# Kernel tuning notes

Hardware: AMD Instinct MI355X
Metric: run time of the kernel (lower is better)

The kernel has to match this reference:

```python
import jax, jax.numpy as jnp
import numpy as np

B, S, D, H = 2, 2048, 2048, 32
HD = D // H  # head_dim = 64
ROPE_BASE = 10000.0


def setup_inputs() -> dict:
    key = jax.random.key(0)
    ks = jax.random.split(key, 5)
    x = jax.random.normal(ks[0], (B, S, D), jnp.float32)
    wq = jax.random.normal(ks[1], (D, D), jnp.float32) * 0.02
    wk = jax.random.normal(ks[2], (D, D), jnp.float32) * 0.02
    wv = jax.random.normal(ks[3], (D, D), jnp.float32) * 0.02
    wo = jax.random.normal(ks[4], (D, D), jnp.float32) * 0.02
    # RoPE frequencies, same as llama precompute_freqs_cis: (S, HD//2)
    inv_freq = 1.0 / (ROPE_BASE ** (jnp.arange(0, HD, 2, dtype=jnp.float32) / HD))
    freqs = jnp.outer(jnp.arange(S, dtype=jnp.float32), inv_freq)
    freqs_cos = jnp.cos(freqs)
    freqs_sin = jnp.sin(freqs)
    # additive causal mask (1,1,S,S): 0 on/below diagonal, -1e9 above
    mask = jnp.where(jnp.tril(jnp.ones((S, S), bool)), 0.0, -1e9).astype(jnp.float32)[None, None]
    return {"x": x, "wq": wq, "wk": wk, "wv": wv, "wo": wo,
            "freqs_cos": freqs_cos, "freqs_sin": freqs_sin, "mask": mask}


def _rope(t, cos, sin):
    # t: [b, s, h, d]; cos/sin: [s, d//2]; interleaved complex rotation
    tr, ti = t[..., 0::2], t[..., 1::2]
    c = cos[None, :, None, :]
    s = sin[None, :, None, :]
    out_r = tr * c - ti * s
    out_i = tr * s + ti * c
    return jnp.stack([out_r, out_i], axis=-1).reshape(t.shape)


def reference(x, wq, wk, wv, wo, freqs_cos, freqs_sin, mask):
    b, s, _ = x.shape
    q = (x @ wq).reshape(b, s, H, HD)
    k = (x @ wk).reshape(b, s, H, HD)
    v = (x @ wv).reshape(b, s, H, HD)
    q = _rope(q, freqs_cos, freqs_sin)
    k = _rope(k, freqs_cos, freqs_sin)
    # [b, h, s, d]
    q = q.transpose(0, 2, 1, 3)
    k = k.transpose(0, 2, 1, 3)
    v = v.transpose(0, 2, 1, 3)
    scores = jnp.einsum('bhqd,bhkd->bhqk', q, k) / np.sqrt(HD).astype(np.float32)
    scores = scores + mask
    probs = jax.nn.softmax(scores.astype(jnp.float32), axis=-1).astype(q.dtype)
    out = jnp.einsum('bhqk,bhkd->bhqd', probs, v)
    out = out.transpose(0, 2, 1, 3).reshape(b, s, H * HD)
    return out @ wo
```

## Files before the change

### kernel.cpp

```cpp
#include <hip/hip_runtime.h>
#include <hip/hip_bf16.h>
#include <stdint.h>

typedef unsigned short u16;
typedef __attribute__((ext_vector_type(4))) float f32x4;
typedef __attribute__((ext_vector_type(8))) short s16x8;
typedef __attribute__((ext_vector_type(4))) short s16x4;

#define B_  2
#define S_  2048
#define D_  2048
#define H_  32
#define HD_ 64

static __device__ __forceinline__ float bf2f(u16 u) {
    union { uint32_t i; float f; } v; v.i = ((uint32_t)u) << 16; return v.f;
}
static __device__ __forceinline__ u16 f2bf(float f) {
    union { float f; uint32_t i; } v; v.f = f;
    uint32_t r = v.i + 0x7FFFu + ((v.i >> 16) & 1u);
    return (u16)(r >> 16);
}
static __device__ __forceinline__ bool probe_f32(const u16* fc) {
    return *(const uint32_t*)fc == 0x3F800000u;
}
static __device__ __forceinline__ void gload_lds16(const void* g, void* l) {
    __builtin_amdgcn_global_load_lds(
        (const __attribute__((address_space(1))) uint32_t*)g,
        (__attribute__((address_space(3))) uint32_t*)l, 16, 0, 0);
}

__global__ __launch_bounds__(256) void k_cast_x(const void* __restrict__ in,
    const u16* __restrict__ fc, u16* __restrict__ out)
{
    const bool f32 = probe_f32(fc);
    const size_t i = ((size_t)blockIdx.x * 256 + threadIdx.x) * 8;
    if (f32) {
        const float* inf = (const float*)in;
        f32x4 lo = *(const f32x4*)(inf + i);
        f32x4 hi = *(const f32x4*)(inf + i + 4);
        s16x8 o;
        #pragma unroll
        for (int j = 0; j < 4; ++j) {
            o[j]     = (short)f2bf(lo[j]);
            o[4 + j] = (short)f2bf(hi[j]);
        }
        *(s16x8*)(out + i) = o;
    } else {
        *(s16x8*)(out + i) = *(const s16x8*)((const u16*)in + i);
    }
}

#define G4_NT 32

static __device__ __forceinline__ void gemm_pipe_body(
    const u16* __restrict__ A, const u16* __restrict__ Bt,
    void* __restrict__ Cv, const int c_f32, const int N,
    const int brow, const int bcol,
    u16 (*__restrict__ AB)[24576])
{
    const int tid = threadIdx.x;
    const int lane = tid & 63;
    const int w = tid >> 6;
    const int wr = w >> 2, wc = w & 3;
    const int l15 = lane & 15, l4 = lane >> 4;
    const int K = 2048;

    f32x4 acc[8][2];
    #pragma unroll
    for (int m = 0; m < 8; ++m)
        #pragma unroll
        for (int n = 0; n < 2; ++n)
            acc[m][n] = (f32x4){0.f, 0.f, 0.f, 0.f};

    auto STAGE = [&](int b, int t) {
        u16* buf = AB[b];
        const int kt = t * 64;
        #pragma unroll
        for (int i = 0; i < 4; ++i) {
            const int ca = i * 512 + tid;
            const int row = ca >> 3, cc = ca & 7;
            const int ccs = cc ^ (row & 7);
            gload_lds16(A + (size_t)(brow + row) * K + kt + ccs * 8,
                        buf + (size_t)(i * 512 + (tid & ~63)) * 8);
        }
        #pragma unroll
        for (int i = 0; i < 2; ++i) {
            const int cb = i * 512 + tid;
            const int row = cb >> 3, cc = cb & 7;
            const int ccs = cc ^ (row & 7);
            gload_lds16(Bt + (size_t)(bcol + row) * K + kt + ccs * 8,
                        buf + 16384 + (size_t)(i * 512 + (tid & ~63)) * 8);
        }
    };

    auto COMPUTE = [&](int b) {
        const u16* Ad = AB[b];
        const u16* Bd = AB[b] + 16384;
        #pragma unroll
        for (int kk = 0; kk < 2; ++kk) {
            s16x8 af[8], bf[2];
            #pragma unroll
            for (int m = 0; m < 8; ++m) {
                const int row = wr * 128 + m * 16 + l15;
                af[m] = *(const s16x8*)(Ad + row * 64 + (((kk * 4 + l4) ^ (row & 7)) << 3));
            }
            #pragma unroll
            for (int n = 0; n < 2; ++n) {
                const int row = wc * 32 + n * 16 + l15;
                bf[n] = *(const s16x8*)(Bd + row * 64 + (((kk * 4 + l4) ^ (row & 7)) << 3));
            }
            #pragma unroll
            for (int m = 0; m < 8; ++m)
                #pragma unroll
                for (int n = 0; n < 2; ++n)
                    acc[m][n] = __builtin_amdgcn_mfma_f32_16x16x32_bf16(af[m], bf[n], acc[m][n], 0, 0, 0);
        }
    };

    STAGE(0, 0);
    STAGE(1, 1);
    for (int t = 0; t < G4_NT; ++t) {
        if (t < G4_NT - 1) asm volatile("s_waitcnt vmcnt(6)" ::: "memory");
        else               asm volatile("s_waitcnt vmcnt(0)" ::: "memory");
        __builtin_amdgcn_s_barrier();
        if (t + 2 < G4_NT) STAGE((t + 2) % 3, t + 2);
        COMPUTE(t % 3);
    }

    #pragma unroll
    for (int m = 0; m < 8; ++m) {
        const int row = brow + wr * 128 + m * 16 + l4 * 4;
        #pragma unroll
        for (int n = 0; n < 2; ++n) {
            const int col = bcol + wc * 32 + n * 16 + l15;
            #pragma unroll
            for (int r = 0; r < 4; ++r) {
                if (c_f32)
                    ((float*)Cv)[(size_t)(row + r) * N + col] = acc[m][n][r];
                else
                    ((u16*)Cv)[(size_t)(row + r) * N + col] = f2bf(acc[m][n][r]);
            }
        }
    }
}

__global__ __launch_bounds__(512, 2) void k_gemm_qkv(const u16* __restrict__ xb,
    const u16* __restrict__ wqt, const u16* __restrict__ wkt, const u16* __restrict__ wvt,
    u16* __restrict__ Q, u16* __restrict__ Kc, u16* __restrict__ V)
{
    __shared__ u16 AB[3][24576];
    const int lin = blockIdx.x + 16 * (blockIdx.y + 16 * blockIdx.z);
    const int swz = (lin & 7) * 96 + (lin >> 3);
    const int bx = swz & 15, by = (swz >> 4) & 15, bz = swz >> 8;
    const u16* Bt = (bz == 0) ? wqt : (bz == 1) ? wkt : wvt;
    u16* C = (bz == 0) ? Q : (bz == 1) ? Kc : V;
    gemm_pipe_body(xb, Bt, C, 0, D_, by * 256, bx * 128, AB);
}

__global__ __launch_bounds__(512, 2) void k_gemm_out(const u16* __restrict__ A,
    const u16* __restrict__ Bt, const u16* __restrict__ fc, void* __restrict__ C)
{
    __shared__ u16 AB[3][24576];
    const int f32 = probe_f32(fc) ? 1 : 0;
    const int lin = blockIdx.x + 16 * blockIdx.y;
    const int swz = (lin & 7) * 32 + (lin >> 3);
    const int bx = swz & 15, by = swz >> 4;
    gemm_pipe_body(A, Bt, C, f32, D_, by * 256, bx * 128, AB);
}

__global__ __launch_bounds__(256) void k_prep_w(const void* __restrict__ in,
    const u16* __restrict__ fc, u16* __restrict__ out)
{
    __shared__ u16 t[64][72];
    const bool f32 = probe_f32(fc);
    const int tid = threadIdx.x;
    const int r0 = blockIdx.y * 64, c0 = blockIdx.x * 64;
    #pragma unroll
    for (int i = 0; i < 2; ++i) {
        const int chunk = i * 256 + tid;
        const int row = chunk >> 3, cc = chunk & 7;
        if (f32) {
            const float* inf = (const float*)in;
            const size_t off = (size_t)(r0 + row) * 2048 + c0 + cc * 8;
            f32x4 lo = *(const f32x4*)(inf + off);
            f32x4 hi = *(const f32x4*)(inf + off + 4);
            #pragma unroll
            for (int j = 0; j < 4; ++j) {
                t[row][cc * 8 + j]     = f2bf(lo[j]);
                t[row][cc * 8 + 4 + j] = f2bf(hi[j]);
            }
        } else {
            s16x8 v = *(const s16x8*)((const u16*)in + (size_t)(r0 + row) * 2048 + c0 + cc * 8);
            *(s16x8*)&t[row][cc * 8] = v;
        }
    }
    __syncthreads();
    #pragma unroll
    for (int i = 0; i < 2; ++i) {
        const int chunk = i * 256 + tid;
        const int orow = chunk >> 3, occ = chunk & 7;
        s16x8 v;
        #pragma unroll
        for (int j = 0; j < 8; ++j) v[j] = (short)t[occ * 8 + j][orow];
        *(s16x8*)(out + (size_t)(c0 + orow) * 2048 + r0 + occ * 8) = v;
    }
}

__global__ __launch_bounds__(256) void k_rope_layout(const u16* __restrict__ Q,
    const u16* __restrict__ K, const u16* __restrict__ V,
    const u16* __restrict__ fc, const u16* __restrict__ fs,
    u16* __restrict__ Qr, u16* __restrict__ Kr, u16* __restrict__ Vt)
{
    __shared__ u16 vt[64][72];
    const bool f32 = probe_f32(fc);
    const float QS = 0.125f * 1.4426950408889634f;
    const int tid = threadIdx.x;
    const int s0 = blockIdx.x * 64;
    const int head = blockIdx.y;
    const int b = head >> 5, h = head & 31;
    const size_t hb = (size_t)head * S_ * HD_;
    #pragma unroll
    for (int i = 0; i < 2; ++i) {
        const int chunk = i * 256 + tid;
        const int sr = chunk >> 3, cc = chunk & 7;
        const int s = s0 + sr;
        const size_t src = ((size_t)(b * S_ + s)) * D_ + h * HD_ + cc * 8;
        float c[4], sn[4];
        if (f32) {
            const float* fcf = (const float*)fc;
            const float* fsf = (const float*)fs;
            #pragma unroll
            for (int j = 0; j < 4; ++j) {
                c[j]  = fcf[s * 32 + cc * 4 + j];
                sn[j] = fsf[s * 32 + cc * 4 + j];
            }
        } else {
            #pragma unroll
            for (int j = 0; j < 4; ++j) {
                c[j]  = bf2f(fc[s * 32 + cc * 4 + j]);
                sn[j] = bf2f(fs[s * 32 + cc * 4 + j]);
            }
        }
        s16x8 vq = *(const s16x8*)(Q + src);
        s16x8 vk = *(const s16x8*)(K + src);
        s16x8 oq, ok;
        #pragma unroll
        for (int j = 0; j < 4; ++j) {
            float qr = bf2f((u16)vq[2 * j]), qi = bf2f((u16)vq[2 * j + 1]);
            oq[2 * j]     = (short)f2bf((qr * c[j] - qi * sn[j]) * QS);
            oq[2 * j + 1] = (short)f2bf((qr * sn[j] + qi * c[j]) * QS);
            float kr = bf2f((u16)vk[2 * j]), ki = bf2f((u16)vk[2 * j + 1]);
            ok[2 * j]     = (short)f2bf(kr * c[j] - ki * sn[j]);
            ok[2 * j + 1] = (short)f2bf(kr * sn[j] + ki * c[j]);
        }
        *(s16x8*)(Qr + hb + (size_t)s * HD_ + cc * 8) = oq;
        *(s16x8*)(Kr + hb + (size_t)s * HD_ + cc * 8) = ok;
        s16x8 vv = *(const s16x8*)(V + src);
        *(s16x8*)&vt[sr][cc * 8] = vv;
    }
    __syncthreads();
    #pragma unroll
    for (int i = 0; i < 2; ++i) {
        const int chunk = i * 256 + tid;
        const int hd = chunk >> 3, sc = chunk & 7;
        s16x8 v;
        #pragma unroll
        for (int j = 0; j < 8; ++j) v[j] = (short)vt[sc * 8 + j][hd];
        *(s16x8*)(Vt + hb + (size_t)hd * S_ + s0 + sc * 8) = v;
    }
}

__global__ __launch_bounds__(512, 2) void k_flash(const u16* __restrict__ Qr,
    const u16* __restrict__ Kr, const u16* __restrict__ Vt, u16* __restrict__ O)
{
    __shared__ u16 Ks[2][64][64];
    __shared__ u16 Vs[2][64][64];
    __shared__ u16 p_lds[8][32][72];
    const int tid = threadIdx.x;
    const int lane = tid & 63, w = tid >> 6;
    const int l15 = lane & 15, l4 = lane >> 4;
    const int bxp = blockIdx.x;
    const int stripe = (w < 4) ? bxp : (15 - bxp);
    const int head = blockIdx.y;
    const int b = head >> 5, h = head & 31;
    const size_t hb = (size_t)head * S_ * HD_;
    const u16* Qh = Qr + hb;
    const u16* Kh = Kr + hb;
    const u16* Vh = Vt + hb;
    const int q0 = stripe * 128 + (w & 3) * 32;
    const int td = stripe * 2 + ((w & 3) >> 1);
    const int T  = 2 * (15 - bxp) + 2;

    s16x8 aq[2][2];
    #pragma unroll
    for (int m = 0; m < 2; ++m) {
        aq[m][0] = *(const s16x8*)(Qh + (size_t)(q0 + m * 16 + l15) * 64 + 0  + l4 * 8);
        aq[m][1] = *(const s16x8*)(Qh + (size_t)(q0 + m * 16 + l15) * 64 + 32 + l4 * 8);
    }
    s16x8 vone;
    #pragma unroll
    for (int j = 0; j < 8; ++j) vone[j] = (short)0x3F80;

    f32x4 oac[2][4];
    f32x4 osum[2];
    #pragma unroll
    for (int m = 0; m < 2; ++m) {
        osum[m] = (f32x4){0.f, 0.f, 0.f, 0.f};
        #pragma unroll
        for (int n = 0; n < 4; ++n) oac[m][n] = (f32x4){0.f, 0.f, 0.f, 0.f};
    }

    const int srow = tid >> 3;
    const int sc8  = tid & 7;

    {
        s16x8 k0 = *(const s16x8*)(Kh + (size_t)srow * 64 + sc8 * 8);
        s16x8 v0 = *(const s16x8*)(Vh + (size_t)srow * S_ + sc8 * 8);
        const int cs = (sc8 ^ (srow & 7)) * 8;
        *(s16x8*)&Ks[0][srow][cs] = k0;
        *(s16x8*)&Vs[0][srow][cs] = v0;
    }

    for (int t = 0; t < T; ++t) {
        const int cb = t & 1;
        __syncthreads();
        s16x8 kn, vn;
        const bool pf = (t + 1 < T);
        if (pf) {
            const int kvn = (t + 1) * 64;
            kn = *(const s16x8*)(Kh + (size_t)(kvn + srow) * 64 + sc8 * 8);
            vn = *(const s16x8*)(Vh + (size_t)srow * S_ + kvn + sc8 * 8);
        }
        if (t <= td) {
            const int kv0 = t * 64;
            const bool masked = (t == td);
            s16x8 bk0[4], bk1[4];
            #pragma unroll
            for (int n = 0; n < 4; ++n) {
                const int row = n * 16 + l15;
                bk0[n] = *(const s16x8*)&Ks[cb][row][((l4      ^ (row & 7)) << 3)];
                bk1[n] = *(const s16x8*)&Ks[cb][row][(((4 + l4) ^ (row & 7)) << 3)];
            }
            f32x4 s4[2][4];
            #pragma unroll
            for (int m = 0; m < 2; ++m)
                #pragma unroll
                for (int n = 0; n < 4; ++n) {
                    f32x4 z = (f32x4){0.f, 0.f, 0.f, 0.f};
                    z = __builtin_amdgcn_mfma_f32_16x16x32_bf16(bk0[n], aq[m][0], z, 0, 0, 0);
                    z = __builtin_amdgcn_mfma_f32_16x16x32_bf16(bk1[n], aq[m][1], z, 0, 0, 0);
                    s4[m][n] = z;
                }
            #pragma unroll
            for (int m = 0; m < 2; ++m)
                #pragma unroll
                for (int n = 0; n < 4; ++n) {
                    s16x4 pk;
                    #pragma unroll
                    for (int r = 0; r < 4; ++r) {
                        float sv = s4[m][n][r];
                        if (masked) {
                            const int kcol = kv0 + n * 16 + l4 * 4 + r;
                            const int qrow = q0 + m * 16 + l15;
                            if (kcol > qrow) sv = -1.0e30f;
                        }
                        pk[r] = (short)f2bf(exp2f(sv));
                    }
                    *(s16x4*)&p_lds[w][m * 16 + l15][n * 16 + l4 * 4] = pk;
                }
            asm volatile("s_waitcnt lgkmcnt(0)" ::: "memory");
            #pragma unroll
            for (int kk = 0; kk < 2; ++kk) {
                s16x8 pa[2];
                #pragma unroll
                for (int m = 0; m < 2; ++m)
                    pa[m] = *(const s16x8*)&p_lds[w][m * 16 + l15][kk * 32 + l4 * 8];
                #pragma unroll
                for (int n = 0; n < 4; ++n) {
                    const int row = n * 16 + l15;
                    s16x8 bv = *(const s16x8*)&Vs[cb][row][(((kk * 4 + l4) ^ (row & 7)) << 3)];
                    #pragma unroll
                    for (int m = 0; m < 2; ++m)
                        oac[m][n] = __builtin_amdgcn_mfma_f32_16x16x32_bf16(pa[m], bv, oac[m][n], 0, 0, 0);
                }
                #pragma unroll
                for (int m = 0; m < 2; ++m)
                    osum[m] = __builtin_amdgcn_mfma_f32_16x16x32_bf16(pa[m], vone, osum[m], 0, 0, 0);
            }
        }
        if (pf) {
            const int nb = cb ^ 1;
            const int cs = (sc8 ^ (srow & 7)) * 8;
            *(s16x8*)&Ks[nb][srow][cs] = kn;
            *(s16x8*)&Vs[nb][srow][cs] = vn;
        }
    }

    #pragma unroll
    for (int m = 0; m < 2; ++m)
        #pragma unroll
        for (int r = 0; r < 4; ++r) {
            const float rl = 1.0f / osum[m][r];
            const int qrow = q0 + m * 16 + l4 * 4 + r;
            #pragma unroll
            for (int n = 0; n < 4; ++n)
                O[(size_t)(b * S_ + qrow) * D_ + h * HD_ + n * 16 + l15] = f2bf(oac[m][n][r] * rl);
        }
}

extern "C" void kernel_launch(void* const* d_in, const int* in_sizes, int n_in,
                              void* d_out, int out_size, void* d_ws, size_t ws_size,
                              hipStream_t stream)
{
    const void* x  = d_in[0];
    const void* wq = d_in[1];
    const void* wk = d_in[2];
    const void* wv = d_in[3];
    const void* wo = d_in[4];
    const u16* fc = (const u16*)d_in[5];
    const u16* fs = (const u16*)d_in[6];

    u16* ws = (u16*)d_ws;
    const size_t WSZ = (size_t)D_ * D_;
    const size_t TSZ = (size_t)B_ * S_ * D_;
    u16* wqt = ws;
    u16* wkt = wqt + WSZ;
    u16* wvt = wkt + WSZ;
    u16* wot = wvt + WSZ;
    u16* Qb  = wot + WSZ;
    u16* Kb  = Qb + TSZ;
    u16* Vb  = Kb + TSZ;
    u16* Qr  = Vb + TSZ;
    u16* Kr  = Qr + TSZ;
    u16* Vt  = Kr + TSZ;
    u16* Ob  = Qb;
    u16* xb  = Qr;

    if (ws_size < (4 * WSZ + 6 * TSZ) * sizeof(u16)) return;

    dim3 blk(256);
    dim3 blk512(512);
    k_cast_x<<<dim3((unsigned)(TSZ / 2048)), blk, 0, stream>>>(x, fc, xb);
    k_prep_w<<<dim3(32, 32), blk, 0, stream>>>(wq, fc, wqt);
    k_prep_w<<<dim3(32, 32), blk, 0, stream>>>(wk, fc, wkt);
    k_prep_w<<<dim3(32, 32), blk, 0, stream>>>(wv, fc, wvt);
    k_prep_w<<<dim3(32, 32), blk, 0, stream>>>(wo, fc, wot);
    k_gemm_qkv<<<dim3(16, 16, 3), blk512, 0, stream>>>(xb, wqt, wkt, wvt, Qb, Kb, Vb);
    k_rope_layout<<<dim3(32, 64), blk, 0, stream>>>(Qb, Kb, Vb, fc, fs, Qr, Kr, Vt);
    k_flash<<<dim3(8, 64), blk512, 0, stream>>>(Qr, Kr, Vt, Ob);
    k_gemm_out<<<dim3(16, 16), blk512, 0, stream>>>(Ob, wot, fc, d_out);
}
```

Baseline: 305.4 us.

## Split flash KV tile into halves, skip fully masked half on diagonal

Splits each 64-key tile into two 32-key halves, computing scores, exp and the PV MFMAs per half. On the diagonal tile, even warps skip the second half entirely because it is fully masked, and only the relevant half applies the causal mask. The per-warp P scratch buffer shrinks to a 32-wide row, which lowers LDS use, and the launch-bounds occupancy hint rises from 2 to 6 blocks. The per-half structure adds an extra LDS wait and serialisation point per tile, and the higher occupancy target may force register spills.

New measurement: 517.4 us. 1.69x slower.

```diff
diff --git a/kernel.cpp b/kernel.cpp
--- a/kernel.cpp
+++ b/kernel.cpp
@@ -271,12 +271,12 @@
     }
 }
 
-__global__ __launch_bounds__(512, 2) void k_flash(const u16* __restrict__ Qr,
+__global__ __launch_bounds__(512, 6) void k_flash(const u16* __restrict__ Qr,
     const u16* __restrict__ Kr, const u16* __restrict__ Vt, u16* __restrict__ O)
 {
     __shared__ u16 Ks[2][64][64];
     __shared__ u16 Vs[2][64][64];
-    __shared__ u16 p_lds[8][32][72];
+    __shared__ u16 p_lds[8][32][40];
     const int tid = threadIdx.x;
     const int lane = tid & 63, w = tid >> 6;
     const int l15 = lane & 15, l4 = lane >> 4;
@@ -290,6 +290,7 @@
     const u16* Vh = Vt + hb;
     const int q0 = stripe * 128 + (w & 3) * 32;
     const int td = stripe * 2 + ((w & 3) >> 1);
+    const bool wodd = (w & 1);
     const int T  = 2 * (15 - bxp) + 2;
 
     s16x8 aq[2][2];
@@ -335,51 +336,53 @@
         if (t <= td) {
             const int kv0 = t * 64;
             const bool masked = (t == td);
-            s16x8 bk0[4], bk1[4];
-            #pragma unroll
-            for (int n = 0; n < 4; ++n) {
-                const int row = n * 16 + l15;
-                bk0[n] = *(const s16x8*)&Ks[cb][row][((l4      ^ (row & 7)) << 3)];
-                bk1[n] = *(const s16x8*)&Ks[cb][row][(((4 + l4) ^ (row & 7)) << 3)];
-            }
-            f32x4 s4[2][4];
-            #pragma unroll
-            for (int m = 0; m < 2; ++m)
-                #pragma unroll
-                for (int n = 0; n < 4; ++n) {
-                    f32x4 z = (f32x4){0.f, 0.f, 0.f, 0.f};
-                    z = __builtin_amdgcn_mfma_f32_16x16x32_bf16(bk0[n], aq[m][0], z, 0, 0, 0);
-                    z = __builtin_amdgcn_mfma_f32_16x16x32_bf16(bk1[n], aq[m][1], z, 0, 0, 0);
-                    s4[m][n] = z;
+            #pragma unroll
+            for (int hf = 0; hf < 2; ++hf) {
+                if (masked && !wodd && hf == 1) break;
+                const bool mh = masked && (wodd ? (hf == 1) : (hf == 0));
+                s16x8 bk0[2], bk1[2];
+                #pragma unroll
+                for (int nn = 0; nn < 2; ++nn) {
+                    const int row = (hf * 2 + nn) * 16 + l15;
+                    bk0[nn] = *(const s16x8*)&Ks[cb][row][((l4      ^ (row & 7)) << 3)];
+                    bk1[nn] = *(const s16x8*)&Ks[cb][row][(((4 + l4) ^ (row & 7)) << 3)];
                 }
-            #pragma unroll
-            for (int m = 0; m < 2; ++m)
-                #pragma unroll
-                for (int n = 0; n < 4; ++n) {
-                    s16x4 pk;
+                f32x4 s4[2][2];
+                #pragma unroll
+                for (int m = 0; m < 2; ++m)
                     #pragma unroll
-                    for (int r = 0; r < 4; ++r) {
-                        float sv = s4[m][n][r];
-                        if (masked) {
-                            const int kcol = kv0 + n * 16 + l4 * 4 + r;
-                            const int qrow = q0 + m * 16 + l15;
-                            if (kcol > qrow) sv = -1.0e30f;
+                    for (int nn = 0; nn < 2; ++nn) {
+                        f32x4 z = (f32x4){0.f, 0.f, 0.f, 0.f};
+                        z = __builtin_amdgcn_mfma_f32_16x16x32_bf16(bk0[nn], aq[m][0], z, 0, 0, 0);
+                        z = __builtin_amdgcn_mfma_f32_16x16x32_bf16(bk1[nn], aq[m][1], z, 0, 0, 0);
+                        s4[m][nn] = z;
+                    }
+                #pragma unroll
+                for (int m = 0; m < 2; ++m)
+                    #pragma unroll
+                    for (int nn = 0; nn < 2; ++nn) {
+                        s16x4 pk;
+                        #pragma unroll
+                        for (int r = 0; r < 4; ++r) {
+                            float sv = s4[m][nn][r];
+                            if (mh) {
+                                const int kcol = kv0 + (hf * 2 + nn) * 16 + l4 * 4 + r;
+                                const int qrow = q0 + m * 16 + l15;
+                                if (kcol > qrow) sv = -1.0e30f;
+                            }
+                            pk[r] = (short)f2bf(exp2f(sv));
                         }
-                        pk[r] = (short)f2bf(exp2f(sv));
+                        *(s16x4*)&p_lds[w][m * 16 + l15][nn * 16 + l4 * 4] = pk;
                     }
-                    *(s16x4*)&p_lds[w][m * 16 + l15][n * 16 + l4 * 4] = pk;
-                }
-            asm volatile("s_waitcnt lgkmcnt(0)" ::: "memory");
-            #pragma unroll
-            for (int kk = 0; kk < 2; ++kk) {
+                asm volatile("s_waitcnt lgkmcnt(0)" ::: "memory");
                 s16x8 pa[2];
                 #pragma unroll
                 for (int m = 0; m < 2; ++m)
-                    pa[m] = *(const s16x8*)&p_lds[w][m * 16 + l15][kk * 32 + l4 * 8];
+                    pa[m] = *(const s16x8*)&p_lds[w][m * 16 + l15][l4 * 8];
                 #pragma unroll
                 for (int n = 0; n < 4; ++n) {
                     const int row = n * 16 + l15;
-                    s16x8 bv = *(const s16x8*)&Vs[cb][row][(((kk * 4 + l4) ^ (row & 7)) << 3)];
+                    s16x8 bv = *(const s16x8*)&Vs[cb][row][(((hf * 4 + l4) ^ (row & 7)) << 3)];
                     #pragma unroll
                     for (int m = 0; m < 2; ++m)
                         oac[m][n] = __builtin_amdgcn_mfma_f32_16x16x32_bf16(pa[m], bv, oac[m][n], 0, 0, 0);
```
